# Kernel tuning notes

Hardware: AMD Instinct MI355X
Metric: run time of the kernel (lower is better)

The kernel has to match this reference:

```python
import jax, jax.numpy as jnp
import numpy as np

QLEN, MLEN, BSZ, D_MODEL, N_HEAD, D_HEAD = 1024, 1024, 4, 1024, 16, 64
KLEN = QLEN + MLEN
LN_EPS = 1e-5


def _linear(x, W, b):
    return x @ W + b


def _layer_norm(x, g, b):
    mu = jnp.mean(x, axis=-1, keepdims=True)
    var = jnp.var(x, axis=-1, keepdims=True)
    return (x - mu) * jax.lax.rsqrt(var + LN_EPS) * g + b


def _rel_shift(x):
    # x: [b, n, q, k] -> Transformer-XL rel-shift via zero-pad + reshape trick
    b, n, q, k = x.shape
    x = jnp.pad(x, ((0, 0), (0, 0), (0, 0), (1, 0)))
    x = x.reshape(b, n, k + 1, q)[:, :, 1:, :].reshape(b, n, q, k)
    return x


def setup_inputs() -> dict:
    key = jax.random.key(0)
    ks = jax.random.split(key, 16)
    s = 0.02
    inp = {
        "w": jax.random.normal(ks[0], (QLEN, BSZ, D_MODEL), jnp.float32),
        "r": jax.random.normal(ks[1], (KLEN, D_MODEL), jnp.float32),
        "r_w_bias": jax.random.normal(ks[2], (N_HEAD, D_HEAD), jnp.float32) * s,
        "r_r_bias": jax.random.normal(ks[3], (N_HEAD, D_HEAD), jnp.float32) * s,
        "mems": jax.random.normal(ks[4], (MLEN, BSZ, D_MODEL), jnp.float32),
        "Wq": jax.random.normal(ks[5], (D_MODEL, N_HEAD * D_HEAD), jnp.float32) * s,
        "bq": jnp.zeros((N_HEAD * D_HEAD,), jnp.float32),
        "Wk": jax.random.normal(ks[6], (D_MODEL, N_HEAD * D_HEAD), jnp.float32) * s,
        "bk": jnp.zeros((N_HEAD * D_HEAD,), jnp.float32),
        "Wv": jax.random.normal(ks[7], (D_MODEL, N_HEAD * D_HEAD), jnp.float32) * s,
        "bv": jnp.zeros((N_HEAD * D_HEAD,), jnp.float32),
        "Wr": jax.random.normal(ks[8], (D_MODEL, N_HEAD * D_HEAD), jnp.float32) * s,
        "br": jnp.zeros((N_HEAD * D_HEAD,), jnp.float32),
        "Wo": jax.random.normal(ks[9], (N_HEAD * D_HEAD, D_MODEL), jnp.float32) * s,
        "bo": jnp.zeros((D_MODEL,), jnp.float32),
        "ln_g": jnp.ones((D_MODEL,), jnp.float32),
        "ln_b": jnp.zeros((D_MODEL,), jnp.float32),
    }
    # causal mask with memory: key j visible to query i iff j <= i + MLEN
    inp["attn_mask"] = jnp.arange(KLEN)[None, :] > (jnp.arange(QLEN)[:, None] + MLEN)
    return inp


def reference(w, r, r_w_bias, r_r_bias, mems, Wq, bq, Wk, bk, Wv, bv, Wr, br,
              Wo, bo, ln_g, ln_b, attn_mask):
    qlen, bsz = w.shape[0], w.shape[1]
    scale = 1.0 / (D_HEAD ** 0.5)

    cat = jnp.concatenate([mems, w], axis=0)               # [klen, b, d]
    klen = cat.shape[0]

    q = _linear(cat, Wq, bq)[-qlen:]                       # [q, b, n*d]
    k = _linear(cat, Wk, bk)                               # [k, b, n*d]
    v = _linear(cat, Wv, bv)
    rk = _linear(r, Wr, br)                                # [rlen, n*d]

    q = q.reshape(qlen, bsz, N_HEAD, D_HEAD)
    k = k.reshape(klen, bsz, N_HEAD, D_HEAD)
    v = v.reshape(klen, bsz, N_HEAD, D_HEAD)
    rk = rk.reshape(r.shape[0], N_HEAD, D_HEAD)

    AC = jnp.einsum('ibnd,jbnd->bnij', q + r_w_bias, k)
    BD = jnp.einsum('ibnd,jnd->bnij', q + r_r_bias, rk)
    BD = _rel_shift(BD)

    attn_score = scale * (AC + BD)                          # [b, n, q, k]
    attn_score = jnp.where(attn_mask[None, None, :, :], -jnp.inf, attn_score)
    attn_prob = jax.nn.softmax(attn_score, axis=3)

    attn_vec = jnp.einsum('bnij,jbnd->ibnd', attn_prob, v)
    attn_vec = attn_vec.reshape(qlen, bsz, N_HEAD * D_HEAD)
    attn_out = _linear(attn_vec, Wo, bo)

    return _layer_norm(w + attn_out, ln_g, ln_b)            # post-lnorm path
```

## Files before the change

kernel.cpp:

```cpp
#include <hip/hip_runtime.h>
#include <stdint.h>


typedef unsigned short u16;
typedef unsigned int u32;
typedef __attribute__((ext_vector_type(8))) short s16x8;
typedef __attribute__((ext_vector_type(4))) float f32x4;

typedef const __attribute__((address_space(1))) void gvoid;
typedef __attribute__((address_space(3))) void lvoid;

__device__ __forceinline__ void async16(const u16* g, u16* l) {
  __builtin_amdgcn_global_load_lds((gvoid*)g, (lvoid*)l, 16, 0, 0);
}

__device__ __forceinline__ float b2f(u16 h) {
  union { u32 u; float f; } v; v.u = ((u32)h) << 16; return v.f;
}
__device__ __forceinline__ u16 f2b(float f) {
  union { float f; u32 u; } v; v.f = f; u32 u = v.u;
  return (u16)((u + 0x7FFFu + ((u >> 16) & 1u)) >> 16);
}
__device__ __forceinline__ bool is_bf16(const u16* lng) { return lng[0] == 0x3F80u; }

__device__ __forceinline__ void ld8(const void* p, size_t idx, bool bf, u16* dst) {
  if (bf) {
    *(uint4*)dst = *(const uint4*)((const u16*)p + idx);
  } else {
    const float* f = (const float*)p + idx;
    float4 a = *(const float4*)f;
    float4 c = *(const float4*)(f + 4);
    dst[0] = f2b(a.x); dst[1] = f2b(a.y); dst[2] = f2b(a.z); dst[3] = f2b(a.w);
    dst[4] = f2b(c.x); dst[5] = f2b(c.y); dst[6] = f2b(c.z); dst[7] = f2b(c.w);
  }
}
__device__ __forceinline__ float ldS(const void* p, int idx, bool bf) {
  return bf ? b2f(((const u16*)p)[idx]) : ((const float*)p)[idx];
}

__device__ __forceinline__ void gemm_bt_body(
    u16* As, u16* Bs,
    const void* Alo, const void* Ahi, int splitRow,
    const u16* BT, const void* bias,
    const void* eb0, const void* eb1,
    u16* C0, u16* C1, bool bfin, bool abf,
    int bm, int bnc)
{
  const int t = threadIdx.x;
  const int lane = t & 63, w = t >> 6;
  const int wr = w >> 1, wc = w & 1;
  const int ml = lane & 15, q = lane >> 4;

  f32x4 zero4 = {0.f, 0.f, 0.f, 0.f};
  f32x4 acc[4][4];
#pragma unroll
  for (int i = 0; i < 4; ++i)
#pragma unroll
    for (int j = 0; j < 4; ++j) acc[i][j] = zero4;

  const int srow = t >> 2;
  const int sch  = t & 3;
  const void* aptr[2]; size_t aidx[2]; const u16* bsrc[2];
#pragma unroll
  for (int p = 0; p < 2; ++p) {
    int gr = bm + srow + p * 64;
    if (gr < splitRow) { aptr[p] = Alo; aidx[p] = (size_t)gr * 1024 + sch * 8; }
    else { aptr[p] = Ahi; aidx[p] = (size_t)(gr - splitRow) * 1024 + sch * 8; }
    bsrc[p] = BT + (size_t)(bnc + srow + p * 64) * 1024 + sch * 8;
  }
  u16* lA[2] = { As + t * 8, As + 2048 + t * 8 };
  u16* lB[2] = { Bs + t * 8, Bs + 2048 + t * 8 };

  for (int kk = 0; kk < 1024; kk += 32) {
    if (abf) {
      __syncthreads();
      async16((const u16*)aptr[0] + aidx[0] + kk, lA[0]);
      async16((const u16*)aptr[1] + aidx[1] + kk, lA[1]);
      async16(bsrc[0] + kk, lB[0]);
      async16(bsrc[1] + kk, lB[1]);
      __syncthreads();
    } else {
      u16 ta0[8], ta1[8];
      ld8(aptr[0], aidx[0] + kk, false, ta0);
      ld8(aptr[1], aidx[1] + kk, false, ta1);
      uint4 vb0 = *(const uint4*)(bsrc[0] + kk);
      uint4 vb1 = *(const uint4*)(bsrc[1] + kk);
      __syncthreads();
      *(uint4*)lA[0] = *(uint4*)ta0;
      *(uint4*)lA[1] = *(uint4*)ta1;
      *(uint4*)lB[0] = vb0;
      *(uint4*)lB[1] = vb1;
      __syncthreads();
    }
    s16x8 af[4], bf[4];
#pragma unroll
    for (int mi = 0; mi < 4; ++mi)
      af[mi] = *(const s16x8*)&As[(wr * 64 + mi * 16 + ml) * 32 + q * 8];
#pragma unroll
    for (int ni = 0; ni < 4; ++ni)
      bf[ni] = *(const s16x8*)&Bs[(wc * 64 + ni * 16 + ml) * 32 + q * 8];
#pragma unroll
    for (int mi = 0; mi < 4; ++mi)
#pragma unroll
      for (int ni = 0; ni < 4; ++ni)
        acc[mi][ni] = __builtin_amdgcn_mfma_f32_16x16x32_bf16(af[mi], bf[ni],
                                                              acc[mi][ni], 0, 0, 0);
  }

#pragma unroll
  for (int ni = 0; ni < 4; ++ni) {
    int gcol = bnc + wc * 64 + ni * 16 + ml;
    float bi = ldS(bias, gcol, bfin);
    float e0 = eb0 ? ldS(eb0, gcol, bfin) : 0.f;
    float e1 = eb1 ? ldS(eb1, gcol, bfin) : 0.f;
#pragma unroll
    for (int mi = 0; mi < 4; ++mi)
#pragma unroll
      for (int rr = 0; rr < 4; ++rr) {
        int grow = bm + wr * 64 + mi * 16 + 4 * q + rr;
        size_t off = (size_t)grow * 1024 + gcol;
        float v0 = acc[mi][ni][rr] + bi;
        if (C1) { C0[off] = f2b(v0 + e0); C1[off] = f2b(v0 + e1); }
        else    { C0[off] = f2b(v0); }
      }
  }
}

__device__ __forceinline__ void gemm_vt_body(
    u16* As, u16* Bs,
    const void* Mlo, const void* Whi,
    const u16* WvT, const void* bv,
    u16* vT, bool bfin,
    int j0, int nc0, int b)
{
  const int t = threadIdx.x;
  const int lane = t & 63, w = t >> 6;
  const int wr = w >> 1, wc = w & 1;
  const int ml = lane & 15, q = lane >> 4;

  f32x4 zero4 = {0.f, 0.f, 0.f, 0.f};
  f32x4 acc[4][4];
#pragma unroll
  for (int i = 0; i < 4; ++i)
#pragma unroll
    for (int j = 0; j < 4; ++j) acc[i][j] = zero4;

  const int srow = t >> 2, sch = t & 3;
  const u16* asrc[2]; const void* bptr[2]; size_t bidx[2];
#pragma unroll
  for (int p = 0; p < 2; ++p) {
    asrc[p] = WvT + (size_t)(nc0 + srow + p * 64) * 1024 + sch * 8;
    int j = j0 + srow + p * 64;
    if (j < 1024) { bptr[p] = Mlo; bidx[p] = ((size_t)j * 4 + b) * 1024 + sch * 8; }
    else { bptr[p] = Whi; bidx[p] = ((size_t)(j - 1024) * 4 + b) * 1024 + sch * 8; }
  }
  u16* lA[2] = { As + t * 8, As + 2048 + t * 8 };
  u16* lB[2] = { Bs + t * 8, Bs + 2048 + t * 8 };

  for (int kk = 0; kk < 1024; kk += 32) {
    if (bfin) {
      __syncthreads();
      async16(asrc[0] + kk, lA[0]);
      async16(asrc[1] + kk, lA[1]);
      async16((const u16*)bptr[0] + bidx[0] + kk, lB[0]);
      async16((const u16*)bptr[1] + bidx[1] + kk, lB[1]);
      __syncthreads();
    } else {
      u16 tb0[8], tb1[8];
      ld8(bptr[0], bidx[0] + kk, false, tb0);
      ld8(bptr[1], bidx[1] + kk, false, tb1);
      __syncthreads();
      async16(asrc[0] + kk, lA[0]);
      async16(asrc[1] + kk, lA[1]);
      *(uint4*)lB[0] = *(uint4*)tb0;
      *(uint4*)lB[1] = *(uint4*)tb1;
      __syncthreads();
    }
    s16x8 af[4], bf[4];
#pragma unroll
    for (int mi = 0; mi < 4; ++mi)
      af[mi] = *(const s16x8*)&As[(wr * 64 + mi * 16 + ml) * 32 + q * 8];
#pragma unroll
    for (int ni = 0; ni < 4; ++ni)
      bf[ni] = *(const s16x8*)&Bs[(wc * 64 + ni * 16 + ml) * 32 + q * 8];
#pragma unroll
    for (int mi = 0; mi < 4; ++mi)
#pragma unroll
      for (int ni = 0; ni < 4; ++ni)
        acc[mi][ni] = __builtin_amdgcn_mfma_f32_16x16x32_bf16(af[mi], bf[ni],
                                                              acc[mi][ni], 0, 0, 0);
  }

#pragma unroll
  for (int mi = 0; mi < 4; ++mi)
#pragma unroll
    for (int rr = 0; rr < 4; ++rr) {
      int nc = nc0 + wr * 64 + mi * 16 + 4 * q + rr;
      float bi = ldS(bv, nc, bfin);
      size_t rbase = ((size_t)b * 1024 + nc) * 2048 + j0;
#pragma unroll
      for (int ni = 0; ni < 4; ++ni)
        vT[rbase + wc * 64 + ni * 16 + ml] = f2b(acc[mi][ni][rr] + bi);
    }
}

__global__ __launch_bounds__(256) void gemm_bt(
    const void* __restrict__ Alo, const void* __restrict__ Ahi, int splitRow,
    const u16* __restrict__ BT, const void* __restrict__ bias,
    const void* __restrict__ eb0, const void* __restrict__ eb1,
    u16* __restrict__ C0, u16* __restrict__ C1,
    const u16* __restrict__ lng, int aIsInput)
{
  __shared__ u16 As[128 * 32];
  __shared__ u16 Bs[128 * 32];
  const bool bfin = is_bf16(lng);
  const bool abf = aIsInput ? bfin : true;
  gemm_bt_body(As, Bs, Alo, Ahi, splitRow, BT, bias, eb0, eb1, C0, C1,
               bfin, abf, blockIdx.y * 128, blockIdx.x * 128);
}

__global__ __launch_bounds__(256) void proj_uber(
    const void* __restrict__ mems, const void* __restrict__ w,
    const void* __restrict__ r,
    const u16* __restrict__ WkT, const void* __restrict__ bk,
    const u16* __restrict__ WvT, const void* __restrict__ bv,
    const u16* __restrict__ WqT, const void* __restrict__ bq,
    const void* __restrict__ rwb, const void* __restrict__ rrb,
    const u16* __restrict__ WrT, const void* __restrict__ br,
    u16* __restrict__ kb, u16* __restrict__ vT,
    u16* __restrict__ qw, u16* __restrict__ qr, u16* __restrict__ rkb,
    const u16* __restrict__ lng)
{
  __shared__ u16 As[128 * 32];
  __shared__ u16 Bs[128 * 32];
  const bool bfin = is_bf16(lng);
  int id = blockIdx.x;
  id = (id & 7) * 176 + (id >> 3);

  if (id < 512) {
    int bx = id & 7, by = id >> 3;
    gemm_bt_body(As, Bs, mems, w, 4096, WkT, bk, nullptr, nullptr,
                 kb, nullptr, bfin, bfin, by * 128, bx * 128);
  } else if (id < 1024) {
    int local = id - 512;
    int jx = local & 15, ny = (local >> 4) & 7, b = local >> 7;
    gemm_vt_body(As, Bs, mems, w, WvT, bv, vT, bfin, jx * 128, ny * 128, b);
  } else if (id < 1280) {
    int local = id - 1024;
    int bx = local & 7, by = local >> 3;
    gemm_bt_body(As, Bs, w, w, 4096, WqT, bq, rwb, rrb,
                 qw, qr, bfin, bfin, by * 128, bx * 128);
  } else {
    int local = id - 1280;
    int bx = local & 7, by = local >> 3;
    gemm_bt_body(As, Bs, r, r, 1 << 30, WrT, br, nullptr, nullptr,
                 rkb, nullptr, bfin, bfin, by * 128, bx * 128);
  }
}

__global__ __launch_bounds__(256) void transpose_w5(
    const void* __restrict__ W0, const void* __restrict__ W1,
    const void* __restrict__ W2, const void* __restrict__ W3,
    const void* __restrict__ W4,
    u16* __restrict__ T0, u16* __restrict__ T1, u16* __restrict__ T2,
    u16* __restrict__ T3, u16* __restrict__ T4, const u16* __restrict__ lng)
{
  __shared__ u16 tile[64 * 72];
  const bool bf = is_bf16(lng);
  const void* W; u16* T;
  switch (blockIdx.z) {
    case 0: W = W0; T = T0; break;
    case 1: W = W1; T = T1; break;
    case 2: W = W2; T = T2; break;
    case 3: W = W3; T = T3; break;
    default: W = W4; T = T4; break;
  }
  const int t = threadIdx.x;
  const int k0 = blockIdx.y * 64, n0 = blockIdx.x * 64;
#pragma unroll
  for (int p = 0; p < 2; ++p) {
    int s = p * 256 + t, row = s >> 3, ch = s & 7;
    u16 tmp[8];
    ld8(W, (size_t)(k0 + row) * 1024 + n0 + ch * 8, bf, tmp);
    *(uint4*)&tile[row * 72 + ch * 8] = *(uint4*)tmp;
  }
  __syncthreads();
#pragma unroll
  for (int p = 0; p < 2; ++p) {
    int s = p * 256 + t, nrow = s >> 3, ch = s & 7;
    union { u16 u[8]; uint4 v; } pk;
#pragma unroll
    for (int jj = 0; jj < 8; ++jj) pk.u[jj] = tile[(ch * 8 + jj) * 72 + nrow];
    *(uint4*)(T + (size_t)(n0 + nrow) * 1024 + k0 + ch * 8) = pk.v;
  }
}

__global__ __launch_bounds__(512, 4) void flash_attn(
    const u16* __restrict__ qw, const u16* __restrict__ qr,
    const u16* __restrict__ kb, const u16* __restrict__ vt,
    const u16* __restrict__ rkb, u16* __restrict__ av)
{
  constexpr int LP = 72;
  __shared__ u16 Ks[64 * LP];
  __shared__ u16 Vs[64 * LP];
  __shared__ u16 Rs[192 * LP];
  __shared__ u16 Ps[8][16 * LP];

  const int t = threadIdx.x;
  const int lane = t & 63, w = t >> 6;
  const int ml = lane & 15, q = lane >> 4;
  const int i0 = blockIdx.x * 128;
  const int bn = blockIdx.y, b = bn >> 4, nh = bn & 15;

  s16x8 aqw[2], aqr[2];
  {
    size_t qo = ((size_t)(i0 + 16 * w + ml) * 4 + b) * 1024 + nh * 64 + q * 8;
    aqw[0] = *(const s16x8*)(qw + qo);
    aqw[1] = *(const s16x8*)(qw + qo + 32);
    aqr[0] = *(const s16x8*)(qr + qo);
    aqr[1] = *(const s16x8*)(qr + qo + 32);
  }

  f32x4 zero4 = {0.f, 0.f, 0.f, 0.f};
  f32x4 o[4];
#pragma unroll
  for (int dt = 0; dt < 4; ++dt) o[dt] = zero4;
  float lsum[4] = {0.f, 0.f, 0.f, 0.f};

  const int ntiles = min(i0 / 64 + 18, 32);
  const int c_lo = 16 * (7 - w);
  const int srow = t >> 3, sch = t & 7;

  uint4 pK, pV, pR0, pR1, pR2;
  auto issue = [&](int jt) {
    const int j0n = jt * 64;
    const int jb2 = j0n - i0 + 896;
    pK = *(const uint4*)(kb + ((size_t)(j0n + srow) * 4 + b) * 1024 + nh * 64 + sch * 8);
    pV = *(const uint4*)(vt + ((size_t)bn * 64 + srow) * 2048 + j0n + sch * 8);
    int r0 = jb2 + srow;
    int r1 = r0 + 64;
    int r2 = r0 + 128;
    r0 = r0 < 0 ? 0 : (r0 > 2047 ? 2047 : r0);
    r1 = r1 < 0 ? 0 : (r1 > 2047 ? 2047 : r1);
    r2 = r2 < 0 ? 0 : (r2 > 2047 ? 2047 : r2);
    pR0 = *(const uint4*)(rkb + (size_t)r0 * 1024 + nh * 64 + sch * 8);
    pR1 = *(const uint4*)(rkb + (size_t)r1 * 1024 + nh * 64 + sch * 8);
    pR2 = *(const uint4*)(rkb + (size_t)r2 * 1024 + nh * 64 + sch * 8);
  };
  issue(0);

  for (int jt = 0; jt < ntiles; ++jt) {
    const int j0 = jt * 64;
    __syncthreads();
    *(uint4*)&Ks[srow * LP + sch * 8] = pK;
    *(uint4*)&Vs[srow * LP + sch * 8] = pV;
    *(uint4*)&Rs[(srow      ) * LP + sch * 8] = pR0;
    *(uint4*)&Rs[(srow +  64) * LP + sch * 8] = pR1;
    *(uint4*)&Rs[(srow + 128) * LP + sch * 8] = pR2;
    __syncthreads();
    if (jt + 1 < ntiles) issue(jt + 1);

    f32x4 sac[4];
#pragma unroll
    for (int tt = 0; tt < 4; ++tt) sac[tt] = zero4;
#pragma unroll
    for (int ki = 0; ki < 2; ++ki)
#pragma unroll
      for (int tt = 0; tt < 4; ++tt) {
        s16x8 bfr = *(const s16x8*)&Ks[(tt * 16 + ml) * LP + ki * 32 + q * 8];
        sac[tt] = __builtin_amdgcn_mfma_f32_16x16x32_bf16(aqw[ki], bfr, sac[tt], 0, 0, 0);
      }

    f32x4 g[5];
#pragma unroll
    for (int ct = 0; ct < 5; ++ct) g[ct] = zero4;
#pragma unroll
    for (int ki = 0; ki < 2; ++ki)
#pragma unroll
      for (int ct = 0; ct < 5; ++ct) {
        s16x8 bfr = *(const s16x8*)&Rs[(c_lo + ct * 16 + ml) * LP + ki * 32 + q * 8];
        g[ct] = __builtin_amdgcn_mfma_f32_16x16x32_bf16(aqr[ki], bfr, g[ct], 0, 0, 0);
      }

    const bool mtile = (j0 + 63) > (i0 + 1024);

#pragma unroll
    for (int rr = 0; rr < 4; ++rr) {
      const int r = 4 * q + rr;
      const int irow = i0 + 16 * w + r;
      const int L = ((ml - r + 15) & 15) | (q << 4);
      float h0 = __shfl(g[0][rr], L, 64);
      float h1 = __shfl(g[1][rr], L, 64);
      float h2 = __shfl(g[2][rr], L, 64);
      float h3 = __shfl(g[3][rr], L, 64);
      float h4 = __shfl(g[4][rr], L, 64);
      const bool hi = ml > r;
      float band0 = hi ? h1 : h0, band1 = hi ? h2 : h1;
      float band2 = hi ? h3 : h2, band3 = hi ? h4 : h3;
      float s0 = 0.125f * (sac[0][rr] + band0);
      float s1 = 0.125f * (sac[1][rr] + band1);
      float s2 = 0.125f * (sac[2][rr] + band2);
      float s3 = 0.125f * (sac[3][rr] + band3);
      if (mtile) {
        int lim = irow + 1024 - j0 - ml;
        if (0 > lim)  s0 = -3.0e38f;
        if (16 > lim) s1 = -3.0e38f;
        if (32 > lim) s2 = -3.0e38f;
        if (48 > lim) s3 = -3.0e38f;
      }
      float p0 = __expf(s0), p1 = __expf(s1), p2 = __expf(s2), p3 = __expf(s3);
      lsum[rr] += (p0 + p1) + (p2 + p3);
      Ps[w][r * LP +  0 + ml] = f2b(p0);
      Ps[w][r * LP + 16 + ml] = f2b(p1);
      Ps[w][r * LP + 32 + ml] = f2b(p2);
      Ps[w][r * LP + 48 + ml] = f2b(p3);
    }

#pragma unroll
    for (int ki = 0; ki < 2; ++ki) {
      s16x8 a = *(const s16x8*)&Ps[w][ml * LP + ki * 32 + q * 8];
#pragma unroll
      for (int dt = 0; dt < 4; ++dt) {
        s16x8 bfr = *(const s16x8*)&Vs[(dt * 16 + ml) * LP + ki * 32 + q * 8];
        o[dt] = __builtin_amdgcn_mfma_f32_16x16x32_bf16(a, bfr, o[dt], 0, 0, 0);
      }
    }
  }

#pragma unroll
  for (int rr = 0; rr < 4; ++rr) {
    float l = lsum[rr];
#pragma unroll
    for (int off = 1; off < 16; off <<= 1) l += __shfl_xor(l, off);
    float inv = 1.f / l;
    int i = i0 + 16 * w + 4 * q + rr;
#pragma unroll
    for (int dt = 0; dt < 4; ++dt)
      av[((size_t)i * 4 + b) * 1024 + nh * 64 + dt * 16 + ml] = f2b(o[dt][rr] * inv);
  }
}

__global__ __launch_bounds__(256) void ln_kernel(
    const void* __restrict__ wi, const u16* __restrict__ ao,
    const void* __restrict__ gg, const void* __restrict__ bb,
    void* __restrict__ out)
{
  __shared__ float red[8];
  const bool bf = is_bf16((const u16*)gg);
  const int t = threadIdx.x;
  const int row = blockIdx.x;
  const int base = row * 1024 + t * 4;
  float x0, x1, x2, x3;
  if (bf) {
    ushort4 xw = *(const ushort4*)((const u16*)wi + base);
    x0 = b2f(xw.x); x1 = b2f(xw.y); x2 = b2f(xw.z); x3 = b2f(xw.w);
  } else {
    float4 xw = *(const float4*)((const float*)wi + base);
    x0 = xw.x; x1 = xw.y; x2 = xw.z; x3 = xw.w;
  }
  ushort4 xa = *(const ushort4*)(ao + base);
  x0 += b2f(xa.x); x1 += b2f(xa.y); x2 += b2f(xa.z); x3 += b2f(xa.w);
  float s = x0 + x1 + x2 + x3;
  float s2 = x0 * x0 + x1 * x1 + x2 * x2 + x3 * x3;
#pragma unroll
  for (int off = 1; off < 64; off <<= 1) {
    s += __shfl_xor(s, off);
    s2 += __shfl_xor(s2, off);
  }
  if ((t & 63) == 0) { red[t >> 6] = s; red[4 + (t >> 6)] = s2; }
  __syncthreads();
  float S = red[0] + red[1] + red[2] + red[3];
  float S2 = red[4] + red[5] + red[6] + red[7];
  float mu = S * (1.f / 1024.f);
  float var = S2 * (1.f / 1024.f) - mu * mu;
  float inv = rsqrtf(var + 1e-5f);
  float g0 = ldS(gg, t * 4 + 0, bf), g1 = ldS(gg, t * 4 + 1, bf);
  float g2 = ldS(gg, t * 4 + 2, bf), g3 = ldS(gg, t * 4 + 3, bf);
  float b0 = ldS(bb, t * 4 + 0, bf), b1 = ldS(bb, t * 4 + 1, bf);
  float b2v = ldS(bb, t * 4 + 2, bf), b3 = ldS(bb, t * 4 + 3, bf);
  float y0 = (x0 - mu) * inv * g0 + b0;
  float y1 = (x1 - mu) * inv * g1 + b1;
  float y2 = (x2 - mu) * inv * g2 + b2v;
  float y3 = (x3 - mu) * inv * g3 + b3;
  if (bf) {
    ushort4 r;
    r.x = f2b(y0); r.y = f2b(y1); r.z = f2b(y2); r.w = f2b(y3);
    *(ushort4*)((u16*)out + base) = r;
  } else {
    float4 r; r.x = y0; r.y = y1; r.z = y2; r.w = y3;
    *(float4*)((float*)out + base) = r;
  }
}

__global__ __launch_bounds__(256) void copy_w(
    const void* __restrict__ wi, const u16* __restrict__ lng,
    void* __restrict__ out)
{
  const bool bf = is_bf16(lng);
  int i = blockIdx.x * 256 + threadIdx.x;
  if (bf) ((u16*)out)[i] = ((const u16*)wi)[i];
  else    ((float*)out)[i] = ((const float*)wi)[i];
}

extern "C" void kernel_launch(void* const* d_in, const int* in_sizes, int n_in,
                              void* d_out, int out_size, void* d_ws, size_t ws_size,
                              hipStream_t stream) {
  (void)in_sizes; (void)n_in; (void)out_size;
  const void* w    = d_in[0];
  const void* r    = d_in[1];
  const void* rwb  = d_in[2];
  const void* rrb  = d_in[3];
  const void* mems = d_in[4];
  const void* Wq   = d_in[5];
  const void* bq   = d_in[6];
  const void* Wk   = d_in[7];
  const void* bk   = d_in[8];
  const void* Wv   = d_in[9];
  const void* bv   = d_in[10];
  const void* Wr   = d_in[11];
  const void* br   = d_in[12];
  const void* Wo   = d_in[13];
  const void* bo   = d_in[14];
  const u16*  lng  = (const u16*)d_in[15];
  const void* lnb  = d_in[16];

  dim3 blk(256);
  const size_t M = (size_t)1 << 20;
  const size_t NEED = 31 * M * 2;
  if (ws_size < NEED) {
    copy_w<<<dim3(16384), blk, 0, stream>>>(w, lng, d_out);
    return;
  }

  u16* ws  = (u16*)d_ws;
  u16* WqT = ws + 0 * M;
  u16* WkT = ws + 1 * M;
  u16* WvT = ws + 2 * M;
  u16* WrT = ws + 3 * M;
  u16* WoT = ws + 4 * M;
  u16* kb  = ws + 5 * M;
  u16* vT  = ws + 13 * M;
  u16* qw  = ws + 21 * M;
  u16* qr  = ws + 25 * M;
  u16* rkb = ws + 29 * M;
  u16* av  = ws + 0 * M;
  u16* ao  = qw;

  transpose_w5<<<dim3(16, 16, 5), blk, 0, stream>>>(Wq, Wk, Wv, Wr, Wo,
                                                    WqT, WkT, WvT, WrT, WoT, lng);
  proj_uber<<<dim3(1408), blk, 0, stream>>>(mems, w, r,
                                            WkT, bk, WvT, bv, WqT, bq, rwb, rrb,
                                            WrT, br, kb, vT, qw, qr, rkb, lng);
  flash_attn<<<dim3(8, 64), dim3(512), 0, stream>>>(qw, qr, kb, vT, rkb, av);
  gemm_bt<<<dim3(8, 32), blk, 0, stream>>>(av, av, 1 << 30, WoT, bo,
                                           nullptr, nullptr, ao, nullptr, lng, 0);
  ln_kernel<<<dim3(4096), blk, 0, stream>>>(w, ao, lng, lnb, d_out);
}
```

Measured before the change: 393.5 us.

## Reuse rel-pos key slabs via ring buffer, swizzle blocks, pack P/V stores

The attention kernel now keeps the 192-row relative-position key window in shared memory as a three-slab ring buffer. Each iteration loads only one new 64-row slab instead of reloading all three, which cuts global loads and register staging. The block index is remapped so consecutive blocks share (batch, head) K/V/R data, for better L2 locality. The rel-shift selection now happens before the shuffle, so only four shuffles are needed instead of five. P in shared memory and the transposed V in the GEMM epilogue are written as packed 8-byte stores using a consistent permutation of key positions within each 64-key tile. The risks are correctness of the matching permutation and the ring-buffer index arithmetic.

```diff
diff --git a/kernel.cpp b/kernel.cpp
--- a/kernel.cpp
+++ b/kernel.cpp
@@ -197,10 +197,11 @@
     for (int rr = 0; rr < 4; ++rr) {
       int nc = nc0 + wr * 64 + mi * 16 + 4 * q + rr;
       float bi = ldS(bv, nc, bfin);
-      size_t rbase = ((size_t)b * 1024 + nc) * 2048 + j0;
-#pragma unroll
-      for (int ni = 0; ni < 4; ++ni)
-        vT[rbase + wc * 64 + ni * 16 + ml] = f2b(acc[mi][ni][rr] + bi);
+      size_t rbase = ((size_t)b * 1024 + nc) * 2048 + j0 + wc * 64 + ml * 4;
+      u32 w0 = (u32)f2b(acc[mi][0][rr] + bi) | ((u32)f2b(acc[mi][1][rr] + bi) << 16);
+      u32 w1 = (u32)f2b(acc[mi][2][rr] + bi) | ((u32)f2b(acc[mi][3][rr] + bi) << 16);
+      uint2 pk; pk.x = w0; pk.y = w1;
+      *(uint2*)(vT + rbase) = pk;
     }
 }
 
@@ -309,8 +310,10 @@
   const int t = threadIdx.x;
   const int lane = t & 63, w = t >> 6;
   const int ml = lane & 15, q = lane >> 4;
-  const int i0 = blockIdx.x * 128;
-  const int bn = blockIdx.y, b = bn >> 4, nh = bn & 15;
+  const int hbid = blockIdx.y * 8 + blockIdx.x;
+  const int lbid = (hbid & 7) * 64 + (hbid >> 3);
+  const int i0 = (lbid & 7) * 128;
+  const int bn = lbid >> 3, b = bn >> 4, nh = bn & 15;
 
   s16x8 aqw[2], aqr[2];
   {
@@ -331,34 +334,47 @@
   const int c_lo = 16 * (7 - w);
   const int srow = t >> 3, sch = t & 7;
 
-  uint4 pK, pV, pR0, pR1, pR2;
-  auto issue = [&](int jt) {
+  uint4 pK, pV, pR;
+  auto issue_kv = [&](int jt) {
     const int j0n = jt * 64;
-    const int jb2 = j0n - i0 + 896;
     pK = *(const uint4*)(kb + ((size_t)(j0n + srow) * 4 + b) * 1024 + nh * 64 + sch * 8);
     pV = *(const uint4*)(vt + ((size_t)bn * 64 + srow) * 2048 + j0n + sch * 8);
-    int r0 = jb2 + srow;
-    int r1 = r0 + 64;
-    int r2 = r0 + 128;
-    r0 = r0 < 0 ? 0 : (r0 > 2047 ? 2047 : r0);
-    r1 = r1 < 0 ? 0 : (r1 > 2047 ? 2047 : r1);
-    r2 = r2 < 0 ? 0 : (r2 > 2047 ? 2047 : r2);
-    pR0 = *(const uint4*)(rkb + (size_t)r0 * 1024 + nh * 64 + sch * 8);
-    pR1 = *(const uint4*)(rkb + (size_t)r1 * 1024 + nh * 64 + sch * 8);
-    pR2 = *(const uint4*)(rkb + (size_t)r2 * 1024 + nh * 64 + sch * 8);
   };
-  issue(0);
-
+  auto rload = [&](int g) {
+    g = g < 0 ? 0 : (g > 2047 ? 2047 : g);
+    return *(const uint4*)(rkb + (size_t)g * 1024 + nh * 64 + sch * 8);
+  };
+
+  {
+    issue_kv(0);
+    uint4 r0 = rload(896 - i0 + srow);
+    uint4 r1 = rload(896 - i0 + srow + 64);
+    uint4 r2 = rload(896 - i0 + srow + 128);
+    *(uint4*)&Ks[srow * LP + sch * 8] = pK;
+    *(uint4*)&Vs[srow * LP + sch * 8] = pV;
+    *(uint4*)&Rs[(srow      ) * LP + sch * 8] = r0;
+    *(uint4*)&Rs[(srow +  64) * LP + sch * 8] = r1;
+    *(uint4*)&Rs[(srow + 128) * LP + sch * 8] = r2;
+  }
+  __syncthreads();
+
+  int slab = 0;
+  int rbase = c_lo;
   for (int jt = 0; jt < ntiles; ++jt) {
     const int j0 = jt * 64;
-    __syncthreads();
-    *(uint4*)&Ks[srow * LP + sch * 8] = pK;
-    *(uint4*)&Vs[srow * LP + sch * 8] = pV;
-    *(uint4*)&Rs[(srow      ) * LP + sch * 8] = pR0;
-    *(uint4*)&Rs[(srow +  64) * LP + sch * 8] = pR1;
-    *(uint4*)&Rs[(srow + 128) * LP + sch * 8] = pR2;
-    __syncthreads();
-    if (jt + 1 < ntiles) issue(jt + 1);
+    if (jt > 0) {
+      __syncthreads();
+      *(uint4*)&Ks[srow * LP + sch * 8] = pK;
+      *(uint4*)&Vs[srow * LP + sch * 8] = pV;
+      *(uint4*)&Rs[(slab * 64 + srow) * LP + sch * 8] = pR;
+      slab = slab == 2 ? 0 : slab + 1;
+      rbase += 64; if (rbase >= 192) rbase -= 192;
+      __syncthreads();
+    }
+    if (jt + 1 < ntiles) {
+      issue_kv(jt + 1);
+      pR = rload(64 * jt + 1088 - i0 + srow);
+    }
 
     f32x4 sac[4];
 #pragma unroll
@@ -375,12 +391,14 @@
 #pragma unroll
     for (int ct = 0; ct < 5; ++ct) g[ct] = zero4;
 #pragma unroll
-    for (int ki = 0; ki < 2; ++ki)
-#pragma unroll
-      for (int ct = 0; ct < 5; ++ct) {
-        s16x8 bfr = *(const s16x8*)&Rs[(c_lo + ct * 16 + ml) * LP + ki * 32 + q * 8];
-        g[ct] = __builtin_amdgcn_mfma_f32_16x16x32_bf16(aqr[ki], bfr, g[ct], 0, 0, 0);
-      }
+    for (int ct = 0; ct < 5; ++ct) {
+      int pb = rbase + ct * 16; if (pb >= 192) pb -= 192;
+      const u16* rp = &Rs[(pb + ml) * LP + q * 8];
+      s16x8 b0 = *(const s16x8*)(rp);
+      s16x8 b1 = *(const s16x8*)(rp + 32);
+      g[ct] = __builtin_amdgcn_mfma_f32_16x16x32_bf16(aqr[0], b0, g[ct], 0, 0, 0);
+      g[ct] = __builtin_amdgcn_mfma_f32_16x16x32_bf16(aqr[1], b1, g[ct], 0, 0, 0);
+    }
 
     const bool mtile = (j0 + 63) > (i0 + 1024);
 
@@ -389,14 +407,15 @@
       const int r = 4 * q + rr;
       const int irow = i0 + 16 * w + r;
       const int L = ((ml - r + 15) & 15) | (q << 4);
-      float h0 = __shfl(g[0][rr], L, 64);
-      float h1 = __shfl(g[1][rr], L, 64);
-      float h2 = __shfl(g[2][rr], L, 64);
-      float h3 = __shfl(g[3][rr], L, 64);
-      float h4 = __shfl(g[4][rr], L, 64);
-      const bool hi = ml > r;
-      float band0 = hi ? h1 : h0, band1 = hi ? h2 : h1;
-      float band2 = hi ? h3 : h2, band3 = hi ? h4 : h3;
+      const bool hs = ml < 15 - r;
+      float bl0 = hs ? g[1][rr] : g[0][rr];
+      float bl1 = hs ? g[2][rr] : g[1][rr];
+      float bl2 = hs ? g[3][rr] : g[2][rr];
+      float bl3 = hs ? g[4][rr] : g[3][rr];
+      float band0 = __shfl(bl0, L, 64);
+      float band1 = __shfl(bl1, L, 64);
+      float band2 = __shfl(bl2, L, 64);
+      float band3 = __shfl(bl3, L, 64);
       float s0 = 0.125f * (sac[0][rr] + band0);
       float s1 = 0.125f * (sac[1][rr] + band1);
       float s2 = 0.125f * (sac[2][rr] + band2);
@@ -410,10 +429,10 @@
       }
       float p0 = __expf(s0), p1 = __expf(s1), p2 = __expf(s2), p3 = __expf(s3);
       lsum[rr] += (p0 + p1) + (p2 + p3);
-      Ps[w][r * LP +  0 + ml] = f2b(p0);
-      Ps[w][r * LP + 16 + ml] = f2b(p1);
-      Ps[w][r * LP + 32 + ml] = f2b(p2);
-      Ps[w][r * LP + 48 + ml] = f2b(p3);
+      u32 w0 = (u32)f2b(p0) | ((u32)f2b(p1) << 16);
+      u32 w1 = (u32)f2b(p2) | ((u32)f2b(p3) << 16);
+      uint2 pk; pk.x = w0; pk.y = w1;
+      *(uint2*)&Ps[w][r * LP + ml * 4] = pk;
     }
 
 #pragma unroll
```

New measurement: 368.5 us. -6.4%, faster.
